# Performance work log

Hardware: AMD Instinct MI355X
Metric: run time of the kernel (lower is better)

## Reference

```python
import jax, jax.numpy as jnp
import numpy as np

L, D, A = 3, 128, 64
NREL2 = 2 * 200 + 1
N_NODE, N_EDGE = 100000, 600000
NQ, N_ENT = 512, 50000


def setup_inputs() -> dict:
    key = jax.random.key(0)
    ks = jax.random.split(key, 30)
    s = 0.05
    inp = {
        "rela_embed": jax.random.normal(ks[0], (L, NREL2, D)) * s,
        "Ws": jax.random.normal(ks[1], (L, A, D)) * s,
        "Wr": jax.random.normal(ks[2], (L, A, D)) * s,
        "Wqr_w": jax.random.normal(ks[3], (L, A, D)) * s,
        "Wqr_b": jax.random.normal(ks[4], (L, A)) * s,
        "Wtau": jax.random.normal(ks[5], (L, A, D)) * s,
        "walpha_w": jax.random.normal(ks[6], (L, 1, A)) * s,
        "walpha_b": jax.random.normal(ks[7], (L, 1)) * s,
        "Wh": jax.random.normal(ks[8], (L, D, D)) * s,
        "wt1": jax.random.normal(ks[9], (L, 1, D)) * s,
        "bt1": jax.random.normal(ks[10], (L, 1, D)) * s,
        "wt2": jax.random.normal(ks[11], (L, 1, D)) * s,
        "bt2": jax.random.normal(ks[12], (L, 1, D)) * s,
        "Wih": jax.random.normal(ks[13], (L, 3 * D, D)) * s,
        "Whh": jax.random.normal(ks[14], (L, 3 * D, D)) * s,
        "bih": jax.random.normal(ks[15], (L, 3 * D)) * s,
        "bhh": jax.random.normal(ks[16], (L, 3 * D)) * s,
        "Wfinal": jax.random.normal(ks[17], (D,)) * s,
        "q_rel": jax.random.randint(ks[18], (NQ,), 0, NREL2),
        "q_tau": jax.random.randint(ks[19], (NQ,), 0, 366),
        "edge_ridx": jax.random.randint(ks[20], (L, N_EDGE), 0, NQ),
        "edge_rel": jax.random.randint(ks[21], (L, N_EDGE), 0, NREL2),
        "edge_tau": jax.random.randint(ks[22], (L, N_EDGE), 0, 366),
        "edge_sub": jax.random.randint(ks[23], (L, N_EDGE), 0, N_NODE),
        "edge_obj": jax.random.randint(ks[24], (L, N_EDGE), 0, N_NODE),
        "nodes_batch": jax.random.randint(ks[25], (N_NODE,), 0, NQ),
        "nodes_ent": jax.random.randint(ks[26], (N_NODE,), 0, N_ENT),
        "n_ent": N_ENT,
    }
    return inp


def _gru_cell(x, h, Wih, Whh, bih, bhh):
    # PyTorch GRU cell semantics (seq_len == 1)
    gi = x @ Wih.T + bih  # [N, 3D]
    gh = h @ Whh.T + bhh
    i_r, i_z, i_n = jnp.split(gi, 3, axis=-1)
    h_r, h_z, h_n = jnp.split(gh, 3, axis=-1)
    r = jax.nn.sigmoid(i_r + h_r)
    z = jax.nn.sigmoid(i_z + h_z)
    n = jnp.tanh(i_n + r * h_n)
    return (1.0 - z) * n + z * h


def reference(rela_embed, Ws, Wr, Wqr_w, Wqr_b, Wtau, walpha_w, walpha_b, Wh,
              wt1, bt1, wt2, bt2, Wih, Whh, bih, bhh, Wfinal,
              q_rel, q_tau, edge_ridx, edge_rel, edge_tau, edge_sub, edge_obj,
              nodes_batch, nodes_ent, n_ent):
    n_node = nodes_batch.shape[0]
    nq = q_rel.shape[0]
    d = Wh.shape[-1]
    hidden = jnp.zeros((n_node, d), dtype=rela_embed.dtype)
    h0 = jnp.zeros((n_node, d), dtype=rela_embed.dtype)
    coe_timediff = 0.2  # computed in original but unused downstream

    for l in range(rela_embed.shape[0]):
        sub, rel, obj = edge_sub[l], edge_rel[l], edge_obj[l]
        ridx = edge_ridx[l]
        hs = hidden[sub]                      # [E, D] gather
        hr = rela_embed[l][rel]               # [E, D] embedding gather
        h_qr = rela_embed[l][q_rel][ridx]     # [E, D]
        taus_q = q_tau[ridx]
        tau = jnp.where(edge_tau[l] >= 0, edge_tau[l], taus_q)
        delta = (tau - taus_q).astype(rela_embed.dtype)[:, None]  # [E, 1]
        h_hau = wt1[l] * delta + bt1[l] + jnp.sin(wt2[l] * delta + bt2[l])
        message = hs + hr + h_hau
        attn = jax.nn.relu(hs @ Ws[l].T + hr @ Wr[l].T + h_qr @ Wqr_w[l].T
                           + Wqr_b[l] + h_hau @ Wtau[l].T)  # [E, A]
        alpha = jax.nn.sigmoid(attn @ walpha_w[l].T + walpha_b[l])  # [E, 1]
        msg = alpha * message
        agg = jax.ops.segment_sum(msg, obj, num_segments=n_node)  # scatter-add
        hidden = jax.nn.relu(agg @ Wh[l].T)
        # old_nodes_new_idx == identity here, so index_copy of h0 is passthrough
        h = _gru_cell(hidden, h0, Wih[l], Whh[l], bih[l], bhh[l])
        hidden, h0 = h, h

    scores = hidden @ Wfinal  # [n_node]
    scores_all = jnp.zeros((nq, n_ent), dtype=scores.dtype)
    scores_all = scores_all.at[nodes_batch, nodes_ent].set(scores)
    return scores_all
```

## Files before the change

### kernel.cpp

```cpp
#include <hip/hip_runtime.h>
#include <hip/hip_bf16.h>
#include <math.h>

typedef __hip_bfloat16 bf16;
typedef __attribute__((ext_vector_type(8))) short s8v;
typedef __attribute__((ext_vector_type(4))) float f4v;
typedef __attribute__((ext_vector_type(4))) float f4x;
typedef __attribute__((ext_vector_type(4))) short s4v;

constexpr int Lc = 3, Dc = 128, Ac = 64, NREL2c = 401;
constexpr int NEc = 600000, NNc = 100000, NQc = 512, NENTc = 50000;
constexpr int NTAUc = 731;
constexpr int HBITS = 18;
constexpr unsigned HSIZE = 1u << HBITS, HMASK = HSIZE - 1u;
constexpr int NBLK = (NNc + 255) / 256;

constexpr float SFX = 32767.f, SFXI = 1.f / 32767.f;

constexpr int O_RELA = 0;
constexpr int O_WS   = O_RELA + Lc * NREL2c * Dc;
constexpr int O_WR   = O_WS   + Lc * Ac * Dc;
constexpr int O_WQRW = O_WR   + Lc * Ac * Dc;
constexpr int O_WQRB = O_WQRW + Lc * Ac * Dc;
constexpr int O_WTAU = O_WQRB + Lc * Ac;
constexpr int O_WAW  = O_WTAU + Lc * Ac * Dc;
constexpr int O_WAB  = O_WAW  + Lc * Ac;
constexpr int O_WH   = O_WAB  + Lc;
constexpr int O_WT1  = O_WH   + Lc * Dc * Dc;
constexpr int O_BT1  = O_WT1  + Lc * Dc;
constexpr int O_WT2  = O_BT1  + Lc * Dc;
constexpr int O_BT2  = O_WT2  + Lc * Dc;
constexpr int O_WIH  = O_BT2  + Lc * Dc;
constexpr int O_WHH  = O_WIH  + Lc * 3 * Dc * Dc;
constexpr int O_BIH  = O_WHH  + Lc * 3 * Dc * Dc;
constexpr int O_BHH  = O_BIH  + Lc * 3 * Dc;
constexpr int O_WF   = O_BHH  + Lc * 3 * Dc;
constexpr int NWTAB  = O_WF + Dc;

__device__ const int KOFF[19] = {O_RELA, O_WS, O_WR, O_WQRW, O_WQRB, O_WTAU, O_WAW,
                                 O_WAB, O_WH, O_WT1, O_BT1, O_WT2, O_BT2, O_WIH,
                                 O_WHH, O_BIH, O_BHH, O_WF, NWTAB};

struct Ptrs { const void* p[18]; };

__device__ __forceinline__ float b2f(bf16 x) { return __bfloat162float(x); }
__device__ __forceinline__ float bsf(unsigned short u) {
  return __uint_as_float((unsigned)u << 16);
}
__device__ __forceinline__ float sigm(float x) { return 1.f / (1.f + expf(-x)); }
__device__ __forceinline__ float s2f(short s) { return (float)s * SFXI; }
__device__ __forceinline__ short f2s(float v) { return (short)__float2int_rn(v * SFX); }
__device__ __forceinline__ unsigned short f2b(float v) {
  bf16 h = __float2bfloat16(v);
  return *(unsigned short*)&h;
}
__device__ __forceinline__ f4v mfma16(s8v a, s8v b, f4v c) {
  return __builtin_amdgcn_mfma_f32_16x16x32_bf16(a, b, c, 0, 0, 0);
}

__global__ void detect_dtype(const unsigned* __restrict__ w, int* __restrict__ flag) {
  int lane = threadIdx.x & 63;
  int cnt = 0;
  for (int k = lane; k < 256; k += 64) {
    unsigned e = (w[k] >> 7) & 0xffu;
    cnt += (e >= 96u && e <= 140u) ? 1 : 0;
  }
#pragma unroll
  for (int o = 32; o; o >>= 1) cnt += __shfl_xor(cnt, o, 64);
  if (lane == 0) *flag = (cnt >= 128) ? 0 : 1;
}

__global__ void convert_weights(Ptrs ps, const int* __restrict__ flag,
                                unsigned short* __restrict__ wtab) {
  int idx = blockIdx.x * 256 + threadIdx.x;
  if (idx >= NWTAB) return;
  int b = 0;
  while (idx >= KOFF[b + 1]) ++b;
  int j = idx - KOFF[b];
  unsigned short v;
  if (*flag) v = f2b(((const float*)ps.p[b])[j]);
  else v = ((const unsigned short*)ps.p[b])[j];
  wtab[idx] = v;
}

__global__ void prep_hhau(int l, const bf16* __restrict__ W, float* __restrict__ Hh) {
  int idx = blockIdx.x * 256 + threadIdx.x;
  if (idx >= NTAUc * Dc) return;
  int t = idx >> 7, d = idx & 127;
  float delta = (float)(t - 365);
  Hh[idx] = b2f(W[O_WT1 + l * Dc + d]) * delta + b2f(W[O_BT1 + l * Dc + d]) +
            sinf(b2f(W[O_WT2 + l * Dc + d]) * delta + b2f(W[O_BT2 + l * Dc + d]));
}

__global__ void prep_yr(int l, const bf16* __restrict__ W, float* __restrict__ Yr) {
  int idx = blockIdx.x * 256 + threadIdx.x;
  if (idx >= NREL2c * Ac) return;
  int r = idx >> 6, a = idx & 63;
  const bf16* x = W + O_RELA + (size_t)(l * NREL2c + r) * Dc;
  const bf16* w = W + O_WR + (size_t)(l * Ac + a) * Dc;
  float s = 0.f;
  for (int d = 0; d < Dc; ++d) s = fmaf(b2f(x[d]), b2f(w[d]), s);
  Yr[idx] = s;
}

__global__ void prep_yqr(int l, const bf16* __restrict__ W, const int* __restrict__ q_rel,
                         float* __restrict__ Yqr) {
  int idx = blockIdx.x * 256 + threadIdx.x;
  if (idx >= NQc * Ac) return;
  int q = idx >> 6, a = idx & 63;
  const bf16* x = W + O_RELA + (size_t)(l * NREL2c + q_rel[q]) * Dc;
  const bf16* w = W + O_WQRW + (size_t)(l * Ac + a) * Dc;
  float s = b2f(W[O_WQRB + l * Ac + a]);
  for (int d = 0; d < Dc; ++d) s = fmaf(b2f(x[d]), b2f(w[d]), s);
  Yqr[idx] = s;
}

__global__ void prep_yh(int l, const float* __restrict__ Hh, const bf16* __restrict__ W,
                        float* __restrict__ Yh) {
  int idx = blockIdx.x * 256 + threadIdx.x;
  if (idx >= NTAUc * Ac) return;
  int t = idx >> 6, a = idx & 63;
  const float* x = Hh + (size_t)t * Dc;
  const bf16* w = W + O_WTAU + (size_t)(l * Ac + a) * Dc;
  float s = 0.f;
  for (int d = 0; d < Dc; ++d) s = fmaf(x[d], b2f(w[d]), s);
  Yh[idx] = s;
}

__global__ void k_count(const int* __restrict__ e_obj, int base, int* __restrict__ cnt) {
  int e = blockIdx.x * 256 + threadIdx.x;
  if (e < NEc) atomicAdd(&cnt[e_obj[base + e]], 1);
}

__global__ void k_scan1(const int* __restrict__ cnt, int* __restrict__ bsum) {
  __shared__ int s[256];
  int t = threadIdx.x, g = blockIdx.x * 256 + t;
  s[t] = g < NNc ? cnt[g] : 0;
  __syncthreads();
  for (int o = 128; o > 0; o >>= 1) {
    if (t < o) s[t] += s[t + o];
    __syncthreads();
  }
  if (t == 0) bsum[blockIdx.x] = s[0];
}

__global__ void k_scan2(const int* __restrict__ bsum, int* __restrict__ bpre,
                        int* __restrict__ offsets) {
  if (threadIdx.x == 0) {
    int run = 0;
    for (int i = 0; i < NBLK; ++i) { bpre[i] = run; run += bsum[i]; }
    offsets[NNc] = run;
  }
}

__global__ void k_scan3(const int* __restrict__ cnt, const int* __restrict__ bpre,
                        int* __restrict__ offsets, int* __restrict__ cursor) {
  __shared__ int s[256];
  int t = threadIdx.x, g = blockIdx.x * 256 + t;
  int c = g < NNc ? cnt[g] : 0;
  s[t] = c;
  __syncthreads();
  for (int o = 1; o < 256; o <<= 1) {
    int v = (t >= o) ? s[t - o] : 0;
    __syncthreads();
    s[t] += v;
    __syncthreads();
  }
  if (g < NNc) {
    int off = s[t] - c + bpre[blockIdx.x];
    offsets[g] = off;
    cursor[g] = off;
  }
}

__global__ void k_fill(const int* __restrict__ e_obj, int base, int* __restrict__ cursor,
                       int* __restrict__ eidx) {
  int e = blockIdx.x * 256 + threadIdx.x;
  if (e < NEc) {
    int pos = atomicAdd(&cursor[e_obj[base + e]], 1);
    eidx[pos] = e;
  }
}

__global__ __launch_bounds__(256, 2) void alpha_kernel(
    int l, const bf16* __restrict__ W, const int* __restrict__ e_sub,
    const int* __restrict__ e_rel, const int* __restrict__ e_ridx,
    const int* __restrict__ e_tau, const int* __restrict__ q_tau,
    const short* __restrict__ state, const float* __restrict__ Yr,
    const float* __restrict__ Yqr, const float* __restrict__ Yh,
    float* __restrict__ alphab, unsigned short* __restrict__ dixb) {
  const int tid = threadIdx.x, lane = tid & 63, w = tid >> 6;
  const int col = lane & 15, quad = lane >> 4;
  const unsigned short* Wu = (const unsigned short*)W;
  s8v Bf[4][4];
  if (l != 0) {
#pragma unroll
    for (int kt = 0; kt < 4; ++kt)
#pragma unroll
      for (int ct = 0; ct < 4; ++ct)
        Bf[kt][ct] =
            *(const s8v*)&Wu[O_WS + (size_t)(l * Ac + ct * 16 + col) * Dc + kt * 32 + quad * 8];
  }
  float wa[4];
#pragma unroll
  for (int ct = 0; ct < 4; ++ct) wa[ct] = b2f(W[O_WAW + l * Ac + ct * 16 + col]);
  const float wb = b2f(W[O_WAB + l]);
  const int base = l * NEc;
  const int gw0 = blockIdx.x * 4 + w, nw = gridDim.x * 4;
  for (int g = gw0; g < NEc / 16; g += nw) {
    int e0 = g * 16;
    int sub16 = e_sub[base + e0 + col];
    int rel16 = e_rel[base + e0 + col];
    int ridx16 = e_ridx[base + e0 + col];
    int et16 = e_tau[base + e0 + col];
    int tq16 = q_tau[ridx16];
    int dix16 = ((et16 >= 0) ? et16 : tq16) - tq16 + 365;
    if (lane < 16) dixb[e0 + lane] = (unsigned short)dix16;
    f4v acc[4];
#pragma unroll
    for (int ct = 0; ct < 4; ++ct) acc[ct] = (f4v)0.f;
    if (l != 0) {
#pragma unroll
      for (int kt = 0; kt < 4; ++kt) {
        const short* sp = &state[(size_t)sub16 * Dc + kt * 32 + quad * 8];
        s8v raw = *(const s8v*)sp;
        s8v a;
#pragma unroll
        for (int j = 0; j < 8; ++j) a[j] = (short)f2b((float)raw[j] * SFXI);
#pragma unroll
        for (int ct = 0; ct < 4; ++ct) acc[ct] = mfma16(a, Bf[kt][ct], acc[ct]);
      }
    }
    float sums[4];
#pragma unroll
    for (int r = 0; r < 4; ++r) {
      int m = quad * 4 + r;
      int rel_m = __shfl(rel16, m, 64);
      int ridx_m = __shfl(ridx16, m, 64);
      int dix_m = __shfl(dix16, m, 64);
      float s = 0.f;
#pragma unroll
      for (int ct = 0; ct < 4; ++ct) {
        int a = ct * 16 + col;
        float v = acc[ct][r] + Yr[rel_m * Ac + a] + Yqr[ridx_m * Ac + a] + Yh[dix_m * Ac + a];
        s = fmaf(fmaxf(v, 0.f), wa[ct], s);
      }
      s += __shfl_xor(s, 1, 64);
      s += __shfl_xor(s, 2, 64);
      s += __shfl_xor(s, 4, 64);
      s += __shfl_xor(s, 8, 64);
      sums[r] = s;
    }
    int rr = col - quad * 4;
    if (rr >= 0 && rr < 4) alphab[e0 + col] = sigm(sums[rr] + wb);
  }
}

__global__ __launch_bounds__(256) void gather_kernel(
    int l, const bf16* __restrict__ W, const int* __restrict__ offsets,
    const int* __restrict__ eidx, const float* __restrict__ alphab,
    const unsigned short* __restrict__ dixb, const int* __restrict__ e_sub,
    const int* __restrict__ e_rel, const short* __restrict__ state,
    const float* __restrict__ Hh, float* __restrict__ agg) {
  const int lane = threadIdx.x & 63;
  const int gw = (blockIdx.x * 256 + threadIdx.x) >> 6;
  const int nw = (gridDim.x * 256) >> 6;
  const int base = l * NEc;
  for (int i = gw; i < NNc; i += nw) {
    float a0 = 0.f, a1 = 0.f;
    int s = offsets[i], en = offsets[i + 1];
    for (int p = s; p < en; ++p) {
      int e = eidx[p];
      float al = alphab[e];
      int sub = e_sub[base + e];
      int rel = e_rel[base + e];
      int dix = dixb[e];
      float hs0 = s2f(state[(size_t)sub * Dc + lane]);
      float hs1 = s2f(state[(size_t)sub * Dc + 64 + lane]);
      const bf16* hrp = W + O_RELA + (size_t)(l * NREL2c + rel) * Dc;
      a0 = fmaf(al, hs0 + b2f(hrp[lane]) + Hh[dix * Dc + lane], a0);
      a1 = fmaf(al, hs1 + b2f(hrp[64 + lane]) + Hh[dix * Dc + 64 + lane], a1);
    }
    agg[(size_t)i * Dc + lane] = a0;
    agg[(size_t)i * Dc + 64 + lane] = a1;
  }
}

__global__ __launch_bounds__(256, 2) void node_update(
    int l, const bf16* __restrict__ W, const float* __restrict__ agg,
    short* __restrict__ state) {
  __shared__ __align__(16) unsigned short ldsAhi[64][136];
  __shared__ __align__(16) unsigned short ldsAlo[64][136];
  __shared__ __align__(16) unsigned short ldsH[64][136];
  const int tid = threadIdx.x;
  const int n0 = blockIdx.x * 64;
  for (int e = tid; e < 64 * 32; e += 256) {
    int i = e >> 5, c = (e & 31) * 4;
    int node = n0 + i;
    f4x av = (f4x)0.f;
    s4v hv4 = (s4v)0;
    if (node < NNc) {
      av = __builtin_nontemporal_load((const f4x*)&agg[(size_t)node * Dc + c]);
      hv4 = *(const s4v*)&state[(size_t)node * Dc + c];
    }
    s4v hi4, lo4, hb4;
#pragma unroll
    for (int j = 0; j < 4; ++j) {
      unsigned short hi = f2b(av[j]);
      hi4[j] = (short)hi;
      lo4[j] = (short)f2b(av[j] - bsf(hi));
      hb4[j] = (short)f2b(s2f(hv4[j]));
    }
    *(s4v*)&ldsAhi[i][c] = hi4;
    *(s4v*)&ldsAlo[i][c] = lo4;
    *(s4v*)&ldsH[i][c] = hb4;
  }
  __syncthreads();
  const int lane = tid & 63;
  const int w = tid >> 6;
  const int col = lane & 15;
  const int quad = lane >> 4;
  const int kb = quad * 8;
  const unsigned short* Wu = (const unsigned short*)W;

  f4v xo[2][4];
#pragma unroll
  for (int c = 0; c < 2; ++c)
#pragma unroll
    for (int mt = 0; mt < 4; ++mt) xo[c][mt] = (f4v)0.f;
#pragma unroll
  for (int kt = 0; kt < 4; ++kt) {
    int ko = kt * 32 + kb;
    s8v b0 = *(const s8v*)&Wu[O_WH + (size_t)(l * Dc + w * 16 + col) * Dc + ko];
    s8v b1 = *(const s8v*)&Wu[O_WH + (size_t)(l * Dc + (w + 4) * 16 + col) * Dc + ko];
#pragma unroll
    for (int mt = 0; mt < 4; ++mt) {
      s8v ahi = *(const s8v*)&ldsAhi[mt * 16 + col][ko];
      s8v alo = *(const s8v*)&ldsAlo[mt * 16 + col][ko];
      xo[0][mt] = mfma16(ahi, b0, xo[0][mt]);
      xo[0][mt] = mfma16(alo, b0, xo[0][mt]);
      xo[1][mt] = mfma16(ahi, b1, xo[1][mt]);
      xo[1][mt] = mfma16(alo, b1, xo[1][mt]);
    }
  }
  __syncthreads();
#pragma unroll
  for (int c = 0; c < 2; ++c) {
    int t = w + 4 * c;
#pragma unroll
    for (int mt = 0; mt < 4; ++mt) {
#pragma unroll
      for (int r = 0; r < 4; ++r) {
        float x = fmaxf(xo[c][mt][r], 0.f);
        unsigned short hi = f2b(x);
        ldsAhi[mt * 16 + quad * 4 + r][t * 16 + col] = hi;
        ldsAlo[mt * 16 + quad * 4 + r][t * 16 + col] = f2b(x - bsf(hi));
      }
    }
  }
  __syncthreads();

#pragma unroll 1
  for (int hs = 0; hs < 2; ++hs) {
    const int jcol = hs * 64 + w * 16 + col;
    const int R = l * 384 + jcol;
    f4v racc[4], zacc[4], niacc[4], nhacc[4];
#pragma unroll
    for (int mt = 0; mt < 4; ++mt) {
      racc[mt] = (f4v)0.f;
      zacc[mt] = (f4v)0.f;
      niacc[mt] = (f4v)0.f;
      nhacc[mt] = (f4v)0.f;
    }
#pragma unroll
    for (int kt = 0; kt < 4; ++kt) {
      int ko = kt * 32 + kb;
      s8v bir = *(const s8v*)&Wu[O_WIH + (size_t)R * Dc + ko];
      s8v bhr = *(const s8v*)&Wu[O_WHH + (size_t)R * Dc + ko];
      s8v biz = *(const s8v*)&Wu[O_WIH + (size_t)(R + 128) * Dc + ko];
      s8v bhz = *(const s8v*)&Wu[O_WHH + (size_t)(R + 128) * Dc + ko];
      s8v bin = *(const s8v*)&Wu[O_WIH + (size_t)(R + 256) * Dc + ko];
      s8v bhn = *(const s8v*)&Wu[O_WHH + (size_t)(R + 256) * Dc + ko];
#pragma unroll
      for (int mt = 0; mt < 4; ++mt) {
        s8v xhi = *(const s8v*)&ldsAhi[mt * 16 + col][ko];
        s8v xlo = *(const s8v*)&ldsAlo[mt * 16 + col][ko];
        s8v hf = *(const s8v*)&ldsH[mt * 16 + col][ko];
        racc[mt] = mfma16(xhi, bir, racc[mt]);
        racc[mt] = mfma16(xlo, bir, racc[mt]);
        racc[mt] = mfma16(hf, bhr, racc[mt]);
        zacc[mt] = mfma16(xhi, biz, zacc[mt]);
        zacc[mt] = mfma16(xlo, biz, zacc[mt]);
        zacc[mt] = mfma16(hf, bhz, zacc[mt]);
        niacc[mt] = mfma16(xhi, bin, niacc[mt]);
        niacc[mt] = mfma16(xlo, bin, niacc[mt]);
        nhacc[mt] = mfma16(hf, bhn, nhacc[mt]);
      }
    }
    float bir_ = b2f(W[O_BIH + R]) + b2f(W[O_BHH + R]);
    float biz_ = b2f(W[O_BIH + R + 128]) + b2f(W[O_BHH + R + 128]);
    float bin_ = b2f(W[O_BIH + R + 256]);
    float bhn_ = b2f(W[O_BHH + R + 256]);
#pragma unroll
    for (int mt = 0; mt < 4; ++mt) {
#pragma unroll
      for (int r_ = 0; r_ < 4; ++r_) {
        int node = n0 + mt * 16 + quad * 4 + r_;
        if (node < NNc) {
          float rg = sigm(racc[mt][r_] + bir_);
          float zg = sigm(zacc[mt][r_] + biz_);
          float ng = tanhf(niacc[mt][r_] + bin_ + rg * (nhacc[mt][r_] + bhn_));
          size_t idx = (size_t)node * Dc + jcol;
          float h0 = s2f(state[idx]);
          __builtin_nontemporal_store(f2s((1.f - zg) * ng + zg * h0), &state[idx]);
        }
      }
    }
  }
}

__global__ __launch_bounds__(256) void score_kernel(const short* __restrict__ state,
                                                    const bf16* __restrict__ W,
                                                    float* __restrict__ scores) {
  const int lane = threadIdx.x & 63;
  const int gw = (blockIdx.x * 256 + threadIdx.x) >> 6;
  const int nw = (gridDim.x * 256) >> 6;
  const float w0 = b2f(W[O_WF + lane]), w1 = b2f(W[O_WF + 64 + lane]);
  for (int i = gw; i < NNc; i += nw) {
    float v = s2f(state[(size_t)i * Dc + lane]) * w0 + s2f(state[(size_t)i * Dc + 64 + lane]) * w1;
#pragma unroll
    for (int o = 32; o; o >>= 1) v += __shfl_xor(v, o, 64);
    if (lane == 0) scores[i] = v;
  }
}

__global__ void zero_out(unsigned* __restrict__ out, const int* __restrict__ flag) {
  long words = ((long)NQc * NENTc / 2) * (*flag ? 2 : 1);
  long i = (long)blockIdx.x * 256 + threadIdx.x;
  long stride = (long)gridDim.x * 256;
  for (; i < words; i += stride) out[i] = 0u;
}

__device__ __forceinline__ unsigned hpos(unsigned pos) { return (pos * 2654435761u) >> (32 - HBITS); }

__global__ void scat1(const int* __restrict__ nb, const int* __restrict__ ne,
                      unsigned* __restrict__ hkey, int* __restrict__ hval) {
  int i = blockIdx.x * 256 + threadIdx.x;
  if (i >= NNc) return;
  unsigned pos = (unsigned)(nb[i] * NENTc + ne[i]);
  unsigned key = pos + 1u;
  unsigned h = hpos(pos);
  while (true) {
    unsigned prev = atomicCAS(&hkey[h], 0u, key);
    if (prev == 0u || prev == key) {
      atomicMax(&hval[h], i);
      break;
    }
    h = (h + 1u) & HMASK;
  }
}

__global__ void scat2(const int* __restrict__ nb, const int* __restrict__ ne,
                      const unsigned* __restrict__ hkey, const int* __restrict__ hval,
                      const float* __restrict__ scores, const int* __restrict__ flag,
                      void* __restrict__ out) {
  int i = blockIdx.x * 256 + threadIdx.x;
  if (i >= NNc) return;
  unsigned pos = (unsigned)(nb[i] * NENTc + ne[i]);
  unsigned key = pos + 1u;
  unsigned h = hpos(pos);
  while (true) {
    unsigned k = hkey[h];
    if (k == key) {
      if (hval[h] == i) {
        if (*flag) ((float*)out)[pos] = scores[i];
        else ((bf16*)out)[pos] = __float2bfloat16(scores[i]);
      }
      break;
    }
    if (k == 0u) break;
    h = (h + 1u) & HMASK;
  }
}

extern "C" void kernel_launch(void* const* d_in, const int* in_sizes, int n_in,
                              void* d_out, int out_size, void* d_ws, size_t ws_size,
                              hipStream_t stream) {
  const int* q_rel = (const int*)d_in[18];
  const int* q_tau = (const int*)d_in[19];
  const int* e_ridx = (const int*)d_in[20];
  const int* e_rel = (const int*)d_in[21];
  const int* e_tau = (const int*)d_in[22];
  const int* e_sub = (const int*)d_in[23];
  const int* e_obj = (const int*)d_in[24];
  const int* n_batch = (const int*)d_in[25];
  const int* n_ent_i = (const int*)d_in[26];

  char* p = (char*)d_ws;
  auto alloc = [&](size_t bytes) {
    void* r = (void*)p;
    p += (bytes + 255) & ~(size_t)255;
    return r;
  };
  int* flag = (int*)alloc(256);
  bf16* wtab = (bf16*)alloc((size_t)NWTAB * 2);
  short* state = (short*)alloc((size_t)NNc * Dc * 2);
  char* big = (char*)alloc((size_t)NNc * Dc * 2);
  float* Yr = (float*)big;
  float* Yqr = (float*)(big + 102912);
  float* Hh = (float*)(big + 233984);
  float* Yh = (float*)(big + 608256);
  float* alphab = (float*)(big + 800000);
  unsigned short* dixb = (unsigned short*)(big + 3200000);
  int* cnt = (int*)(big + 4400128);
  int* cursor = (int*)(big + 4800384);
  int* offsets = (int*)(big + 5200640);
  int* bsum = (int*)(big + 5600768);
  int* bpre = (int*)(big + 5602560);
  int* eidx = (int*)(big + 5604352);
  float* scores = (float*)big;
  unsigned* hkey = (unsigned*)(big + 400128);
  int* hval = (int*)(big + 400128 + (size_t)HSIZE * 4);

  float* agg = (float*)d_out;

  detect_dtype<<<1, 64, 0, stream>>>((const unsigned*)d_in[0], flag);
  Ptrs ps;
  for (int i = 0; i < 18; ++i) ps.p[i] = d_in[i];
  convert_weights<<<(NWTAB + 255) / 256, 256, 0, stream>>>(ps, flag, (unsigned short*)wtab);
  hipMemsetAsync(state, 0, (size_t)NNc * Dc * 2, stream);

  for (int l = 0; l < Lc; ++l) {
    hipMemsetAsync(cnt, 0, (size_t)NNc * 4, stream);
    prep_hhau<<<(NTAUc * Dc + 255) / 256, 256, 0, stream>>>(l, wtab, Hh);
    prep_yr<<<(NREL2c * Ac + 255) / 256, 256, 0, stream>>>(l, wtab, Yr);
    prep_yqr<<<(NQc * Ac + 255) / 256, 256, 0, stream>>>(l, wtab, q_rel, Yqr);
    prep_yh<<<(NTAUc * Ac + 255) / 256, 256, 0, stream>>>(l, Hh, wtab, Yh);
    k_count<<<(NEc + 255) / 256, 256, 0, stream>>>(e_obj, l * NEc, cnt);
    k_scan1<<<NBLK, 256, 0, stream>>>(cnt, bsum);
    k_scan2<<<1, 64, 0, stream>>>(bsum, bpre, offsets);
    k_scan3<<<NBLK, 256, 0, stream>>>(cnt, bpre, offsets, cursor);
    k_fill<<<(NEc + 255) / 256, 256, 0, stream>>>(e_obj, l * NEc, cursor, eidx);
    alpha_kernel<<<2048, 256, 0, stream>>>(l, wtab, e_sub, e_rel, e_ridx, e_tau, q_tau,
                                           state, Yr, Yqr, Yh, alphab, dixb);
    gather_kernel<<<2048, 256, 0, stream>>>(l, wtab, offsets, eidx, alphab, dixb, e_sub,
                                            e_rel, state, Hh, agg);
    node_update<<<(NNc + 63) / 64, 256, 0, stream>>>(l, wtab, agg, state);
  }
  score_kernel<<<1024, 256, 0, stream>>>(state, wtab, scores);
  hipMemsetAsync(hkey, 0, (size_t)HSIZE * 4, stream);
  hipMemsetAsync(hval, 0, (size_t)HSIZE * 4, stream);
  zero_out<<<2048, 256, 0, stream>>>((unsigned*)d_out, flag);
  scat1<<<(NNc + 255) / 256, 256, 0, stream>>>(n_batch, n_ent_i, hkey, hval);
  scat2<<<(NNc + 255) / 256, 256, 0, stream>>>(n_batch, n_ent_i, hkey, hval, scores, flag, d_out);
}
```

Baseline: 1.977 ms.

## Skip zero-state work on first layer and loop node tiles per block

On layer 0 the hidden state is all zeros, so the state gather in the edge aggregation, the Whh GEMM and the state loads in the GRU update are skipped. The node update kernel now processes four 64-node tiles per block and keeps the Wh weight fragments in registers across tiles, cutting repeated weight loads and block count. The gain is limited to the first of three layers for the skip, and the persistent tiling raises register pressure and lowers the number of blocks available to fill the GPU.

Measured after the change: 1.892 ms. 4.3% less time.

```diff
diff --git a/kernel.cpp b/kernel.cpp
--- a/kernel.cpp
+++ b/kernel.cpp
@@ -14,6 +14,7 @@
 constexpr int HBITS = 18;
 constexpr unsigned HSIZE = 1u << HBITS, HMASK = HSIZE - 1u;
 constexpr int NBLK = (NNc + 255) / 256;
+constexpr int NTILE = 4;
 
 constexpr float SFX = 32767.f, SFXI = 1.f / 32767.f;
 
@@ -272,11 +273,14 @@
     for (int p = s; p < en; ++p) {
       int e = eidx[p];
       float al = alphab[e];
-      int sub = e_sub[base + e];
       int rel = e_rel[base + e];
       int dix = dixb[e];
-      float hs0 = s2f(state[(size_t)sub * Dc + lane]);
-      float hs1 = s2f(state[(size_t)sub * Dc + 64 + lane]);
+      float hs0 = 0.f, hs1 = 0.f;
+      if (l != 0) {
+        int sub = e_sub[base + e];
+        hs0 = s2f(state[(size_t)sub * Dc + lane]);
+        hs1 = s2f(state[(size_t)sub * Dc + 64 + lane]);
+      }
       const bf16* hrp = W + O_RELA + (size_t)(l * NREL2c + rel) * Dc;
       a0 = fmaf(al, hs0 + b2f(hrp[lane]) + Hh[dix * Dc + lane], a0);
       a1 = fmaf(al, hs1 + b2f(hrp[64 + lane]) + Hh[dix * Dc + 64 + lane], a1);
@@ -293,29 +297,6 @@
   __shared__ __align__(16) unsigned short ldsAlo[64][136];
   __shared__ __align__(16) unsigned short ldsH[64][136];
   const int tid = threadIdx.x;
-  const int n0 = blockIdx.x * 64;
-  for (int e = tid; e < 64 * 32; e += 256) {
-    int i = e >> 5, c = (e & 31) * 4;
-    int node = n0 + i;
-    f4x av = (f4x)0.f;
-    s4v hv4 = (s4v)0;
-    if (node < NNc) {
-      av = __builtin_nontemporal_load((const f4x*)&agg[(size_t)node * Dc + c]);
-      hv4 = *(const s4v*)&state[(size_t)node * Dc + c];
-    }
-    s4v hi4, lo4, hb4;
-#pragma unroll
-    for (int j = 0; j < 4; ++j) {
-      unsigned short hi = f2b(av[j]);
-      hi4[j] = (short)hi;
-      lo4[j] = (short)f2b(av[j] - bsf(hi));
-      hb4[j] = (short)f2b(s2f(hv4[j]));
-    }
-    *(s4v*)&ldsAhi[i][c] = hi4;
-    *(s4v*)&ldsAlo[i][c] = lo4;
-    *(s4v*)&ldsH[i][c] = hb4;
-  }
-  __syncthreads();
   const int lane = tid & 63;
   const int w = tid >> 6;
   const int col = lane & 15;
@@ -323,96 +304,137 @@
   const int kb = quad * 8;
   const unsigned short* Wu = (const unsigned short*)W;
 
-  f4v xo[2][4];
-#pragma unroll
-  for (int c = 0; c < 2; ++c)
-#pragma unroll
-    for (int mt = 0; mt < 4; ++mt) xo[c][mt] = (f4v)0.f;
+  s8v whb[2][4];
 #pragma unroll
   for (int kt = 0; kt < 4; ++kt) {
-    int ko = kt * 32 + kb;
-    s8v b0 = *(const s8v*)&Wu[O_WH + (size_t)(l * Dc + w * 16 + col) * Dc + ko];
-    s8v b1 = *(const s8v*)&Wu[O_WH + (size_t)(l * Dc + (w + 4) * 16 + col) * Dc + ko];
-#pragma unroll
-    for (int mt = 0; mt < 4; ++mt) {
-      s8v ahi = *(const s8v*)&ldsAhi[mt * 16 + col][ko];
-      s8v alo = *(const s8v*)&ldsAlo[mt * 16 + col][ko];
-      xo[0][mt] = mfma16(ahi, b0, xo[0][mt]);
-      xo[0][mt] = mfma16(alo, b0, xo[0][mt]);
-      xo[1][mt] = mfma16(ahi, b1, xo[1][mt]);
-      xo[1][mt] = mfma16(alo, b1, xo[1][mt]);
-    }
-  }
-  __syncthreads();
-#pragma unroll
-  for (int c = 0; c < 2; ++c) {
-    int t = w + 4 * c;
-#pragma unroll
-    for (int mt = 0; mt < 4; ++mt) {
-#pragma unroll
-      for (int r = 0; r < 4; ++r) {
-        float x = fmaxf(xo[c][mt][r], 0.f);
-        unsigned short hi = f2b(x);
-        ldsAhi[mt * 16 + quad * 4 + r][t * 16 + col] = hi;
-        ldsAlo[mt * 16 + quad * 4 + r][t * 16 + col] = f2b(x - bsf(hi));
-      }
-    }
-  }
-  __syncthreads();
+    whb[0][kt] = *(const s8v*)&Wu[O_WH + (size_t)(l * Dc + w * 16 + col) * Dc + kt * 32 + kb];
+    whb[1][kt] =
+        *(const s8v*)&Wu[O_WH + (size_t)(l * Dc + (w + 4) * 16 + col) * Dc + kt * 32 + kb];
+  }
 
 #pragma unroll 1
-  for (int hs = 0; hs < 2; ++hs) {
-    const int jcol = hs * 64 + w * 16 + col;
-    const int R = l * 384 + jcol;
-    f4v racc[4], zacc[4], niacc[4], nhacc[4];
-#pragma unroll
-    for (int mt = 0; mt < 4; ++mt) {
-      racc[mt] = (f4v)0.f;
-      zacc[mt] = (f4v)0.f;
-      niacc[mt] = (f4v)0.f;
-      nhacc[mt] = (f4v)0.f;
-    }
+  for (int tile = 0; tile < NTILE; ++tile) {
+    const int n0 = (blockIdx.x * NTILE + tile) * 64;
+    if (n0 >= NNc) break;
+    if (tile) __syncthreads();
+    for (int e = tid; e < 64 * 32; e += 256) {
+      int i = e >> 5, c = (e & 31) * 4;
+      int node = n0 + i;
+      f4x av = (f4x)0.f;
+      if (node < NNc) av = __builtin_nontemporal_load((const f4x*)&agg[(size_t)node * Dc + c]);
+      s4v hi4, lo4;
+#pragma unroll
+      for (int j = 0; j < 4; ++j) {
+        unsigned short hi = f2b(av[j]);
+        hi4[j] = (short)hi;
+        lo4[j] = (short)f2b(av[j] - bsf(hi));
+      }
+      *(s4v*)&ldsAhi[i][c] = hi4;
+      *(s4v*)&ldsAlo[i][c] = lo4;
+      if (l != 0) {
+        s4v hv4 = (s4v)0, hb4;
+        if (node < NNc) hv4 = *(const s4v*)&state[(size_t)node * Dc + c];
+#pragma unroll
+        for (int j = 0; j < 4; ++j) hb4[j] = (short)f2b(s2f(hv4[j]));
+        *(s4v*)&ldsH[i][c] = hb4;
+      }
+    }
+    __syncthreads();
+
+    f4v xo[2][4];
+#pragma unroll
+    for (int c = 0; c < 2; ++c)
+#pragma unroll
+      for (int mt = 0; mt < 4; ++mt) xo[c][mt] = (f4v)0.f;
 #pragma unroll
     for (int kt = 0; kt < 4; ++kt) {
       int ko = kt * 32 + kb;
-      s8v bir = *(const s8v*)&Wu[O_WIH + (size_t)R * Dc + ko];
-      s8v bhr = *(const s8v*)&Wu[O_WHH + (size_t)R * Dc + ko];
-      s8v biz = *(const s8v*)&Wu[O_WIH + (size_t)(R + 128) * Dc + ko];
-      s8v bhz = *(const s8v*)&Wu[O_WHH + (size_t)(R + 128) * Dc + ko];
-      s8v bin = *(const s8v*)&Wu[O_WIH + (size_t)(R + 256) * Dc + ko];
-      s8v bhn = *(const s8v*)&Wu[O_WHH + (size_t)(R + 256) * Dc + ko];
 #pragma unroll
       for (int mt = 0; mt < 4; ++mt) {
-        s8v xhi = *(const s8v*)&ldsAhi[mt * 16 + col][ko];
-        s8v xlo = *(const s8v*)&ldsAlo[mt * 16 + col][ko];
-        s8v hf = *(const s8v*)&ldsH[mt * 16 + col][ko];
-        racc[mt] = mfma16(xhi, bir, racc[mt]);
-        racc[mt] = mfma16(xlo, bir, racc[mt]);
-        racc[mt] = mfma16(hf, bhr, racc[mt]);
-        zacc[mt] = mfma16(xhi, biz, zacc[mt]);
-        zacc[mt] = mfma16(xlo, biz, zacc[mt]);
-        zacc[mt] = mfma16(hf, bhz, zacc[mt]);
-        niacc[mt] = mfma16(xhi, bin, niacc[mt]);
-        niacc[mt] = mfma16(xlo, bin, niacc[mt]);
-        nhacc[mt] = mfma16(hf, bhn, nhacc[mt]);
-      }
-    }
-    float bir_ = b2f(W[O_BIH + R]) + b2f(W[O_BHH + R]);
-    float biz_ = b2f(W[O_BIH + R + 128]) + b2f(W[O_BHH + R + 128]);
-    float bin_ = b2f(W[O_BIH + R + 256]);
-    float bhn_ = b2f(W[O_BHH + R + 256]);
-#pragma unroll
-    for (int mt = 0; mt < 4; ++mt) {
-#pragma unroll
-      for (int r_ = 0; r_ < 4; ++r_) {
-        int node = n0 + mt * 16 + quad * 4 + r_;
-        if (node < NNc) {
-          float rg = sigm(racc[mt][r_] + bir_);
-          float zg = sigm(zacc[mt][r_] + biz_);
-          float ng = tanhf(niacc[mt][r_] + bin_ + rg * (nhacc[mt][r_] + bhn_));
-          size_t idx = (size_t)node * Dc + jcol;
-          float h0 = s2f(state[idx]);
-          __builtin_nontemporal_store(f2s((1.f - zg) * ng + zg * h0), &state[idx]);
+        s8v ahi = *(const s8v*)&ldsAhi[mt * 16 + col][ko];
+        s8v alo = *(const s8v*)&ldsAlo[mt * 16 + col][ko];
+        xo[0][mt] = mfma16(ahi, whb[0][kt], xo[0][mt]);
+        xo[0][mt] = mfma16(alo, whb[0][kt], xo[0][mt]);
+        xo[1][mt] = mfma16(ahi, whb[1][kt], xo[1][mt]);
+        xo[1][mt] = mfma16(alo, whb[1][kt], xo[1][mt]);
+      }
+    }
+    __syncthreads();
+#pragma unroll
+    for (int c = 0; c < 2; ++c) {
+      int t = w + 4 * c;
+#pragma unroll
+      for (int mt = 0; mt < 4; ++mt) {
+#pragma unroll
+        for (int r = 0; r < 4; ++r) {
+          float x = fmaxf(xo[c][mt][r], 0.f);
+          unsigned short hi = f2b(x);
+          ldsAhi[mt * 16 + quad * 4 + r][t * 16 + col] = hi;
+          ldsAlo[mt * 16 + quad * 4 + r][t * 16 + col] = f2b(x - bsf(hi));
+        }
+      }
+    }
+    __syncthreads();
+
+#pragma unroll 1
+    for (int hs = 0; hs < 2; ++hs) {
+      const int jcol = hs * 64 + w * 16 + col;
+      const int R = l * 384 + jcol;
+      f4v racc[4], zacc[4], niacc[4], nhacc[4];
+#pragma unroll
+      for (int mt = 0; mt < 4; ++mt) {
+        racc[mt] = (f4v)0.f;
+        zacc[mt] = (f4v)0.f;
+        niacc[mt] = (f4v)0.f;
+        nhacc[mt] = (f4v)0.f;
+      }
+#pragma unroll
+      for (int kt = 0; kt < 4; ++kt) {
+        int ko = kt * 32 + kb;
+        s8v bir = *(const s8v*)&Wu[O_WIH + (size_t)R * Dc + ko];
+        s8v biz = *(const s8v*)&Wu[O_WIH + (size_t)(R + 128) * Dc + ko];
+        s8v bin = *(const s8v*)&Wu[O_WIH + (size_t)(R + 256) * Dc + ko];
+#pragma unroll
+        for (int mt = 0; mt < 4; ++mt) {
+          s8v xhi = *(const s8v*)&ldsAhi[mt * 16 + col][ko];
+          s8v xlo = *(const s8v*)&ldsAlo[mt * 16 + col][ko];
+          racc[mt] = mfma16(xhi, bir, racc[mt]);
+          racc[mt] = mfma16(xlo, bir, racc[mt]);
+          zacc[mt] = mfma16(xhi, biz, zacc[mt]);
+          zacc[mt] = mfma16(xlo, biz, zacc[mt]);
+          niacc[mt] = mfma16(xhi, bin, niacc[mt]);
+          niacc[mt] = mfma16(xlo, bin, niacc[mt]);
+        }
+        if (l != 0) {
+          s8v bhr = *(const s8v*)&Wu[O_WHH + (size_t)R * Dc + ko];
+          s8v bhz = *(const s8v*)&Wu[O_WHH + (size_t)(R + 128) * Dc + ko];
+          s8v bhn = *(const s8v*)&Wu[O_WHH + (size_t)(R + 256) * Dc + ko];
+#pragma unroll
+          for (int mt = 0; mt < 4; ++mt) {
+            s8v hf = *(const s8v*)&ldsH[mt * 16 + col][ko];
+            racc[mt] = mfma16(hf, bhr, racc[mt]);
+            zacc[mt] = mfma16(hf, bhz, zacc[mt]);
+            nhacc[mt] = mfma16(hf, bhn, nhacc[mt]);
+          }
+        }
+      }
+      float bir_ = b2f(W[O_BIH + R]) + b2f(W[O_BHH + R]);
+      float biz_ = b2f(W[O_BIH + R + 128]) + b2f(W[O_BHH + R + 128]);
+      float bin_ = b2f(W[O_BIH + R + 256]);
+      float bhn_ = b2f(W[O_BHH + R + 256]);
+#pragma unroll
+      for (int mt = 0; mt < 4; ++mt) {
+#pragma unroll
+        for (int r_ = 0; r_ < 4; ++r_) {
+          int node = n0 + mt * 16 + quad * 4 + r_;
+          if (node < NNc) {
+            float rg = sigm(racc[mt][r_] + bir_);
+            float zg = sigm(zacc[mt][r_] + biz_);
+            float ng = tanhf(niacc[mt][r_] + bin_ + rg * (nhacc[mt][r_] + bhn_));
+            size_t idx = (size_t)node * Dc + jcol;
+            float h0 = (l != 0) ? s2f(state[idx]) : 0.f;
+            __builtin_nontemporal_store(f2s((1.f - zg) * ng + zg * h0), &state[idx]);
+          }
         }
       }
     }
@@ -545,7 +567,7 @@
                                            state, Yr, Yqr, Yh, alphab, dixb);
     gather_kernel<<<2048, 256, 0, stream>>>(l, wtab, offsets, eidx, alphab, dixb, e_sub,
                                             e_rel, state, Hh, agg);
-    node_update<<<(NNc + 63) / 64, 256, 0, stream>>>(l, wtab, agg, state);
+    node_update<<<(NNc + 64 * NTILE - 1) / (64 * NTILE), 256, 0, stream>>>(l, wtab, agg, state);
   }
   score_kernel<<<1024, 256, 0, stream>>>(state, wtab, scores);
   hipMemsetAsync(hkey, 0, (size_t)HSIZE * 4, stream);
```
